# Kernel optimization log

Hardware: AMD Instinct MI355X
Metric: run time of the kernel (lower is better)

Reference implementation:

```python
import jax, jax.numpy as jnp
import numpy as np

TEMP = 0.1
NEG = -1e30  # stands in for removing the diagonal via masked_select
EPS = 1e-12  # F.normalize eps


def _l2norm(x, axis):
    n = jnp.linalg.norm(x, axis=axis, keepdims=True)
    return x / jnp.maximum(n, EPS)


def setup_inputs() -> dict:
    key = jax.random.key(0)
    k = jax.random.split(key, 6)
    B, D = 8192, 128      # instance batch, embed dim
    Bp, P = 256, 256      # patch batch, patches per sample
    v1_ins = jax.random.normal(k[0], (B, D), jnp.float32)
    v2_ins = jax.random.normal(k[1], (B, D), jnp.float32)
    v1_patch = jax.random.normal(k[2], (Bp, D, P), jnp.float32)
    v2_patch = jax.random.normal(k[3], (Bp, D, P), jnp.float32)
    v1_counts = jax.random.randint(k[4], (Bp, P), 0, 50, dtype=jnp.int32)
    v2_counts = jax.random.randint(k[5], (Bp, P), 0, 50, dtype=jnp.int32)
    return {"v1_ins": v1_ins, "v2_ins": v2_ins,
            "v1_patch": v1_patch, "v2_patch": v2_patch,
            "v1_counts": v1_counts, "v2_counts": v2_counts}


def _instance_ce(v1, v2):
    B = v1.shape[0]
    embs = jnp.concatenate([_l2norm(v1, 1), _l2norm(v2, 1)], axis=0)  # [2B, D]
    logits = (embs @ embs.T) / TEMP                                    # [2B, 2B]
    N = 2 * B
    # masking the diagonal to -inf == masked_select removal; positive of row i
    # is column (i+B) mod 2B (matches labels after diagonal removal shift)
    logits = jnp.where(jnp.eye(N, dtype=bool), NEG, logits)
    labels = jnp.concatenate([jnp.arange(B) + B, jnp.arange(B)])
    logp = jax.nn.log_softmax(logits, axis=1)
    return -jnp.mean(logp[jnp.arange(N), labels])


def _patch_ce(v1, v2, c1, c2):
    Bp, D, P = v1.shape
    embs = jnp.concatenate([_l2norm(v1, 1), _l2norm(v2, 1)], axis=2)   # [Bp, D, 2P]
    logits = jnp.einsum('bdi,bdj->bij', embs, embs) / TEMP             # [Bp, 2P, 2P]
    N = 2 * P
    logits = jnp.where(jnp.eye(N, dtype=bool)[None], NEG, logits)
    labels = jnp.concatenate([jnp.arange(P) + P, jnp.arange(P)])       # [2P]
    valid = ~jnp.concatenate([c1 == 0, c2 == 0], axis=1)               # [Bp, 2P]
    logp = jax.nn.log_softmax(logits, axis=2)
    pos = logp[:, jnp.arange(N), labels]                               # [Bp, 2P]
    # ignore_index=-100 -> mean over non-ignored elements
    n_valid = jnp.sum(valid.astype(logits.dtype))
    return -jnp.sum(jnp.where(valid, pos, 0.0)) / n_valid


def reference(v1_ins, v2_ins, v1_patch, v2_patch, v1_counts, v2_counts):
    ins_ce = _instance_ce(v1_ins, v2_ins)
    patch_ce = _patch_ce(v1_patch, v2_patch, v1_counts, v2_counts)
    return ins_ce + patch_ce
```

## Files before the change

### kernel.cpp

```cpp
#include <hip/hip_runtime.h>
#include <math.h>

typedef __bf16 bf16_t;
typedef __bf16 bf16x8 __attribute__((ext_vector_type(8)));
typedef float f32x4 __attribute__((ext_vector_type(4)));
typedef float f32x2 __attribute__((ext_vector_type(2)));

#define B_INS 8192
#define N_INS 16384
#define D 128
#define BP 256
#define P 256
#define NP 512

#define C1_CONST 14.426950408889634f

#define WS_ACC 0
#define WS_S 8
#define WS_POS (8 + 16384)
#define WS_SP (8 + 2 * 16384)
#define WS_PP (WS_SP + BP * NP)
#define WS_ZERO_FLOATS (WS_PP + BP * NP)
#define EMB_I_BYTE ((((WS_ZERO_FLOATS) * 4 + 15) / 16) * 16)
#define EMB_P_BYTE (EMB_I_BYTE + N_INS * D * 2)


#define NB_NORMI 128
#define NB_NORMP 2048
#define NB_ZERO 289
#define NB_PREP (NB_NORMI + NB_NORMP + NB_ZERO)
#define NB_INS 1088
#define NB_PATCHB 1024
#define NB_GRAM (NB_INS + NB_PATCHB)
#define NB_FIN 576

__device__ __forceinline__ void load_lds16(const bf16_t* g, bf16_t* l) {
    __builtin_amdgcn_global_load_lds(
        (const __attribute__((address_space(1))) void*)g,
        (__attribute__((address_space(3))) void*)l, 16, 0, 0);
}

__device__ __forceinline__ void stage_panel(const bf16_t* __restrict__ src,
                                            bf16_t* dst, int w, int lane) {
    const bf16_t* g = src + w * 4096 + lane * 8;
    bf16_t* d = dst + w * 4096;
#pragma unroll
    for (int it = 0; it < 8; it++)
        load_lds16(g + it * 512, d + it * 512);
}

__device__ __forceinline__ void load_afrags(const bf16_t* __restrict__ abase,
                                            int rh, int tx, int q, bf16x8 af[4][4]) {
    const bf16_t* a = abase + ((rh * 64 + tx) << 3);
#pragma unroll
    for (int rt = 0; rt < 4; rt++)
#pragma unroll
        for (int ks = 0; ks < 4; ks++)
            af[rt][ks] = *(const bf16x8*)(a + (((ks << 2) + q) << 10) + (rt << 7));
}

__global__ __launch_bounds__(256) void prep_k(const float* __restrict__ v1i,
                                              const float* __restrict__ v2i,
                                              const float* __restrict__ v1p,
                                              const float* __restrict__ v2p,
                                              bf16_t* __restrict__ embI,
                                              bf16_t* __restrict__ embP,
                                              float* __restrict__ ws) {
    __shared__ float L[128][65];
    __shared__ float ps[4][64];
    __shared__ float invs[128];
    int bx = blockIdx.x;
    int t = threadIdx.x;
    if (bx < NB_NORMI) {
        int p = bx;
        const float* srcP = (p < 64) ? (v1i + (size_t)p * 128 * D)
                                     : (v2i + (size_t)(p - 64) * 128 * D);
        {
            int r = t >> 1, h = t & 1;
            const float* row = srcP + (size_t)r * D + h * 64;
            float ss = 0.f;
#pragma unroll
            for (int j = 0; j < 16; j++) {
                float4 v = *(const float4*)(row + j * 4);
                ss += v.x * v.x + v.y * v.y + v.z * v.z + v.w * v.w;
            }
            ss += __shfl_xor(ss, 1, 64);
            if (h == 0) invs[r] = 1.0f / fmaxf(sqrtf(ss), 1e-12f);
        }
        __syncthreads();
#pragma unroll
        for (int it = 0; it < 8; it++) {
            int idx = it * 256 + t;
            int r = idx & 127, g = idx >> 7;
            const float* src8 = srcP + (size_t)r * D + g * 8;
            float4 a = *(const float4*)(src8);
            float4 b = *(const float4*)(src8 + 4);
            float inv = invs[r];
            bf16x8 v;
            v[0] = (bf16_t)(a.x * inv); v[1] = (bf16_t)(a.y * inv);
            v[2] = (bf16_t)(a.z * inv); v[3] = (bf16_t)(a.w * inv);
            v[4] = (bf16_t)(b.x * inv); v[5] = (bf16_t)(b.y * inv);
            v[6] = (bf16_t)(b.z * inv); v[7] = (bf16_t)(b.w * inv);
            *(bf16x8*)(embI + ((size_t)p << 14) + (g << 10) + (r << 3)) = v;
        }
    } else if (bx < NB_NORMI + NB_NORMP) {
        int bx2 = bx - NB_NORMI;
        int b = bx2 >> 3, h = (bx2 >> 2) & 1, chunk = bx2 & 3;
        int i0 = chunk * 64;
        const float* src = ((h == 0) ? v1p : v2p) + (size_t)b * D * P;
#pragma unroll
        for (int it = 0; it < 8; it++) {
            int fi = it * 256 + t;
            int d = fi >> 4, c4 = fi & 15;
            float4 v = *(const float4*)(src + (size_t)d * P + i0 + c4 * 4);
            L[d][c4 * 4 + 0] = v.x;
            L[d][c4 * 4 + 1] = v.y;
            L[d][c4 * 4 + 2] = v.z;
            L[d][c4 * 4 + 3] = v.w;
        }
        __syncthreads();
        {
            int col = t & 63, part = t >> 6;
            float ss = 0.f;
#pragma unroll 8
            for (int d = part * 32; d < part * 32 + 32; d++) { float x = L[d][col]; ss += x * x; }
            ps[part][col] = ss;
        }
        __syncthreads();
        if (t < 64) {
            float n2 = ps[0][t] + ps[1][t] + ps[2][t] + ps[3][t];
            invs[t] = 1.0f / fmaxf(sqrtf(n2), 1e-12f);
        }
        __syncthreads();
#pragma unroll
        for (int it = 0; it < 4; it++) {
            int idx = it * 256 + t;
            int ic = idx & 63, g = idx >> 6;
            float inv = invs[ic];
            bf16x8 v;
#pragma unroll
            for (int j = 0; j < 8; j++) v[j] = (bf16_t)(L[g * 8 + j][ic] * inv);
            int iLoc = h * P + i0 + ic;
            *(bf16x8*)(embP + ((size_t)b << 16) + ((size_t)(iLoc >> 7) << 14) +
                       (g << 10) + ((iLoc & 127) << 3)) = v;
        }
    } else {
        int idx = (bx - NB_NORMI - NB_NORMP) * 256 + t;
        if (idx < WS_ZERO_FLOATS / 4)
            ((f32x4*)ws)[idx] = (f32x4){0.f, 0.f, 0.f, 0.f};
    }
}

__global__ __launch_bounds__(256) void gram_k(const bf16_t* __restrict__ embI,
                                              const bf16_t* __restrict__ embP,
                                              float* __restrict__ S,
                                              float* __restrict__ pos,
                                              float* __restrict__ Sp,
                                              float* __restrict__ posp) {
    __shared__ __align__(16) bf16_t shB[2][16384];
    int t = threadIdx.x, w = t >> 6, lane = t & 63;
    int tx = lane & 15, q = lane >> 4;
    int rh = w & 1, ch = w >> 1;
    int bx = blockIdx.x;

    const bf16_t *Abase, *Bbase;
    float *Sarr, *posArr;
    int R, c0, n, diagC, posC;
    if (bx < NB_INS) {
        int bid = bx, k = 0, cum = 0;
        while (bid >= cum + 8 * (16 - k)) { cum += 8 * (16 - k); k++; }
        int rem = bid - cum, cc = 16 - k;
        R = 8 * k + rem / cc;
        int ci = rem - (rem / cc) * cc;
        c0 = R + ci * 8;
        n = min(8, 128 - c0);
        Abase = embI + ((size_t)R << 14);
        Bbase = embI;
        Sarr = S; posArr = pos;
        diagC = R; posC = R + 64;
    } else {
        int pi = bx - NB_INS;
        int b = pi >> 2; R = pi & 3;
        c0 = R; n = 4 - R;
        const bf16_t* base = embP + ((size_t)b << 16);
        Abase = base + ((size_t)R << 14);
        Bbase = base;
        Sarr = Sp + (size_t)b * NP; posArr = posp + (size_t)b * NP;
        diagC = R; posC = R + 2;
    }
    int rowBase = R * 128;

    bf16x8 af[4][4];
    load_afrags(Abase, rh, tx, q, af);

    f32x2 rowS2[8];
#pragma unroll
    for (int i = 0; i < 8; i++) rowS2[i] = (f32x2){0.f, 0.f};

    stage_panel(Bbase + ((size_t)c0 << 14), shB[0], w, lane);
    int cur = 0;
    for (int ti = 0; ti < n; ti++) {
        int C = c0 + ti;
        __syncthreads();
        if (ti + 1 < n)
            stage_panel(Bbase + ((size_t)(C + 1) << 14), shB[cur ^ 1], w, lane);
        bool isDiag = (C == diagC), isPos = (C == posC);
        int colBase = C * 128;
        const bf16_t* sb = shB[cur];

        float colS[4];
#pragma unroll
        for (int nt = 0; nt < 4; nt++) {
            bf16x8 bf[4];
#pragma unroll
            for (int ks = 0; ks < 4; ks++)
                bf[ks] = *(const bf16x8*)(sb + (((ks << 2) + q) << 10) +
                                          ((ch * 64 + nt * 16 + tx) << 3));
            f32x4 acc[4];
#pragma unroll
            for (int rt = 0; rt < 4; rt++) acc[rt] = (f32x4){0.f, 0.f, 0.f, 0.f};
#pragma unroll
            for (int ks = 0; ks < 4; ks++)
#pragma unroll
                for (int rt = 0; rt < 4; rt++)
                    acc[rt] = __builtin_amdgcn_mfma_f32_16x16x32_bf16(
                        af[rt][ks], bf[ks], acc[rt], 0, 0, 0);

            f32x2 cs = (f32x2){0.f, 0.f};
#pragma unroll
            for (int rt = 0; rt < 4; rt++) {
                f32x2 l0 = {acc[rt][0], acc[rt][1]};
                f32x2 l1 = {acc[rt][2], acc[rt][3]};
                l0 = l0 * C1_CONST - C1_CONST;
                l1 = l1 * C1_CONST - C1_CONST;
                f32x2 e0 = {__builtin_amdgcn_exp2f(l0.x), __builtin_amdgcn_exp2f(l0.y)};
                f32x2 e1 = {__builtin_amdgcn_exp2f(l1.x), __builtin_amdgcn_exp2f(l1.y)};
                if (isDiag) {
                    int inRow = rh * 64 + rt * 16 + q * 4;
                    int inCol = ch * 64 + nt * 16 + tx;
                    if (inRow + 0 == inCol) e0.x = 0.f;
                    if (inRow + 1 == inCol) e0.y = 0.f;
                    if (inRow + 2 == inCol) e1.x = 0.f;
                    if (inRow + 3 == inCol) e1.y = 0.f;
                }
                rowS2[rt * 2] += e0;
                rowS2[rt * 2 + 1] += e1;
                cs += e0 + e1;
            }
            colS[nt] = cs.x + cs.y;

            if (isPos && ch == rh) {
                int reg = tx - q * 4;
                if (reg >= 0 && reg < 4) {
                    float pl = acc[nt][reg] * 10.0f;
                    atomicAdd(&posArr[rowBase + rh * 64 + nt * 16 + tx], pl);
                    atomicAdd(&posArr[colBase + rh * 64 + nt * 16 + tx], pl);
                }
            }
        }
        if (!isDiag) {
#pragma unroll
            for (int i = 0; i < 4; i++) {
                colS[i] += __shfl_xor(colS[i], 16, 64);
                colS[i] += __shfl_xor(colS[i], 32, 64);
            }
            if (q == 0) {
#pragma unroll
                for (int nt = 0; nt < 4; nt++)
                    atomicAdd(&Sarr[colBase + ch * 64 + nt * 16 + tx], colS[nt]);
            }
        }
        cur ^= 1;
    }
    float* rowS = (float*)rowS2;
#pragma unroll
    for (int off = 1; off <= 8; off <<= 1)
#pragma unroll
        for (int i = 0; i < 16; i++) rowS[i] += __shfl_xor(rowS[i], off, 16);
    if (tx == 0) {
#pragma unroll
        for (int rt = 0; rt < 4; rt++)
#pragma unroll
            for (int reg = 0; reg < 4; reg++)
                atomicAdd(&Sarr[rowBase + rh * 64 + rt * 16 + q * 4 + reg],
                          rowS[rt * 4 + reg]);
    }
}

__global__ __launch_bounds__(256) void fin_k(const float* __restrict__ S,
                                             const float* __restrict__ pos,
                                             const float* __restrict__ Sp,
                                             const float* __restrict__ posp,
                                             const int* __restrict__ c1,
                                             const int* __restrict__ c2,
                                             float* __restrict__ acc,
                                             float* __restrict__ out) {
    int bx = blockIdx.x, t = threadIdx.x;
    int lane = t & 63, w = t >> 6;
    float va = 0.f, nv = 0.f;
    if (bx < 64) {
        int i = bx * 256 + t;
        va = __logf(S[i]) + 10.0f - pos[i];
    } else {
        int idx = (bx - 64) * 256 + t;
        int b = idx >> 9, i = idx & 511;
        int cnt = (i < P) ? c1[b * P + i] : c2[b * P + i - P];
        bool valid = (cnt != 0);
        va = valid ? (__logf(Sp[idx]) + 10.0f - posp[idx]) : 0.f;
        nv = valid ? 1.0f : 0.0f;
    }
#pragma unroll
    for (int off = 32; off >= 1; off >>= 1) {
        va += __shfl_down(va, off, 64);
        nv += __shfl_down(nv, off, 64);
    }
    __shared__ float ps[4], pn[4];
    if (lane == 0) { ps[w] = va; pn[w] = nv; }
    __syncthreads();
    if (t == 0) {
        float sv = ps[0] + ps[1] + ps[2] + ps[3];
        float sn = pn[0] + pn[1] + pn[2] + pn[3];
        if (bx < 64) {
            atomicAdd(&acc[0], sv);
        } else {
            atomicAdd(&acc[1], sv);
            atomicAdd(&acc[2], sn);
        }
        __threadfence();
        unsigned old = atomicAdd((unsigned*)&acc[3], 1u);
        if (old == NB_FIN - 1) {
            float a0 = atomicAdd(&acc[0], 0.0f);
            float a1 = atomicAdd(&acc[1], 0.0f);
            float a2 = atomicAdd(&acc[2], 0.0f);
            out[0] = a0 * (1.0f / (float)N_INS) + a1 / a2;
        }
    }
}

extern "C" void kernel_launch(void* const* d_in, const int* in_sizes, int n_in,
                              void* d_out, int out_size, void* d_ws, size_t ws_size,
                              hipStream_t stream) {
    const float* v1i = (const float*)d_in[0];
    const float* v2i = (const float*)d_in[1];
    const float* v1p = (const float*)d_in[2];
    const float* v2p = (const float*)d_in[3];
    const int* c1 = (const int*)d_in[4];
    const int* c2 = (const int*)d_in[5];
    float* ws = (float*)d_ws;
    float* out = (float*)d_out;
    bf16_t* embI = (bf16_t*)((char*)d_ws + EMB_I_BYTE);
    bf16_t* embP = (bf16_t*)((char*)d_ws + EMB_P_BYTE);

    prep_k<<<NB_PREP, 256, 0, stream>>>(v1i, v2i, v1p, v2p, embI, embP, ws);
    gram_k<<<NB_GRAM, 256, 0, stream>>>(embI, embP, ws + WS_S, ws + WS_POS,
                                        ws + WS_SP, ws + WS_PP);
    fin_k<<<NB_FIN, 256, 0, stream>>>(ws + WS_S, ws + WS_POS, ws + WS_SP,
                                      ws + WS_PP, c1, c2, ws + WS_ACC, out);
}
```

Before: 220.9 us.

## Load B fragments directly from global memory, drop LDS staging and barriers

Removes the double-buffered LDS panel staging and its per-tile __syncthreads, so each wave reads its B fragments straight from global memory (via L2/cache). Adds a launch-bounds occupancy hint of 3 blocks, swizzles the block index so consecutive blocks spread across work regions, and raises wave priority around the MFMA sequence. The aim is to eliminate barrier stalls and raise occupancy now that no LDS is used. The risk is more global-load latency being exposed and redundant B reads across waves that previously shared one LDS copy.

```diff
diff --git a/kernel.cpp b/kernel.cpp
--- a/kernel.cpp
+++ b/kernel.cpp
@@ -33,21 +33,6 @@
 #define NB_PATCHB 1024
 #define NB_GRAM (NB_INS + NB_PATCHB)
 #define NB_FIN 576
-
-__device__ __forceinline__ void load_lds16(const bf16_t* g, bf16_t* l) {
-    __builtin_amdgcn_global_load_lds(
-        (const __attribute__((address_space(1))) void*)g,
-        (__attribute__((address_space(3))) void*)l, 16, 0, 0);
-}
-
-__device__ __forceinline__ void stage_panel(const bf16_t* __restrict__ src,
-                                            bf16_t* dst, int w, int lane) {
-    const bf16_t* g = src + w * 4096 + lane * 8;
-    bf16_t* d = dst + w * 4096;
-#pragma unroll
-    for (int it = 0; it < 8; it++)
-        load_lds16(g + it * 512, d + it * 512);
-}
 
 __device__ __forceinline__ void load_afrags(const bf16_t* __restrict__ abase,
                                             int rh, int tx, int q, bf16x8 af[4][4]) {
@@ -151,17 +136,17 @@
     }
 }
 
-__global__ __launch_bounds__(256) void gram_k(const bf16_t* __restrict__ embI,
-                                              const bf16_t* __restrict__ embP,
-                                              float* __restrict__ S,
-                                              float* __restrict__ pos,
-                                              float* __restrict__ Sp,
-                                              float* __restrict__ posp) {
-    __shared__ __align__(16) bf16_t shB[2][16384];
+__global__ __launch_bounds__(256, 3) void gram_k(const bf16_t* __restrict__ embI,
+                                                 const bf16_t* __restrict__ embP,
+                                                 float* __restrict__ S,
+                                                 float* __restrict__ pos,
+                                                 float* __restrict__ Sp,
+                                                 float* __restrict__ posp) {
     int t = threadIdx.x, w = t >> 6, lane = t & 63;
     int tx = lane & 15, q = lane >> 4;
     int rh = w & 1, ch = w >> 1;
-    int bx = blockIdx.x;
+    int bx0 = blockIdx.x;
+    int bx = (bx0 & 7) * (NB_GRAM / 8) + (bx0 >> 3);
 
     const bf16_t *Abase, *Bbase;
     float *Sarr, *posArr;
@@ -197,16 +182,13 @@
 #pragma unroll
     for (int i = 0; i < 8; i++) rowS2[i] = (f32x2){0.f, 0.f};
 
-    stage_panel(Bbase + ((size_t)c0 << 14), shB[0], w, lane);
-    int cur = 0;
+    const bf16_t* bcol = Bbase + ((size_t)q << 10) + ((ch * 64 + tx) << 3);
+
     for (int ti = 0; ti < n; ti++) {
         int C = c0 + ti;
-        __syncthreads();
-        if (ti + 1 < n)
-            stage_panel(Bbase + ((size_t)(C + 1) << 14), shB[cur ^ 1], w, lane);
         bool isDiag = (C == diagC), isPos = (C == posC);
         int colBase = C * 128;
-        const bf16_t* sb = shB[cur];
+        const bf16_t* pb = bcol + ((size_t)C << 14);
 
         float colS[4];
 #pragma unroll
@@ -214,17 +196,18 @@
             bf16x8 bf[4];
 #pragma unroll
             for (int ks = 0; ks < 4; ks++)
-                bf[ks] = *(const bf16x8*)(sb + (((ks << 2) + q) << 10) +
-                                          ((ch * 64 + nt * 16 + tx) << 3));
+                bf[ks] = *(const bf16x8*)(pb + (ks << 12) + (nt << 7));
             f32x4 acc[4];
 #pragma unroll
             for (int rt = 0; rt < 4; rt++) acc[rt] = (f32x4){0.f, 0.f, 0.f, 0.f};
+            __builtin_amdgcn_s_setprio(1);
 #pragma unroll
             for (int ks = 0; ks < 4; ks++)
 #pragma unroll
                 for (int rt = 0; rt < 4; rt++)
                     acc[rt] = __builtin_amdgcn_mfma_f32_16x16x32_bf16(
                         af[rt][ks], bf[ks], acc[rt], 0, 0, 0);
+            __builtin_amdgcn_s_setprio(0);
 
             f32x2 cs = (f32x2){0.f, 0.f};
 #pragma unroll
@@ -270,7 +253,6 @@
                     atomicAdd(&Sarr[colBase + ch * 64 + nt * 16 + tx], colS[nt]);
             }
         }
-        cur ^= 1;
     }
     float* rowS = (float*)rowS2;
 #pragma unroll
```

Result: slower. 236.1 us (+6.9%).

## Replace global atomic row/column sum accumulation with per-tile partial buffers

Applied to the files above, without the earlier changes.

Instead of atomically adding row and column exp-sums into shared global arrays, each gram tile now writes its partial sums into a dedicated slot. The finalize kernel then reduces these partials per row. This removes atomic contention and the large workspace zeroing in the prep kernel. In exchange it needs more workspace traffic and longer serial reduction loops in the finalize kernel.

```diff
diff --git a/kernel.cpp b/kernel.cpp
--- a/kernel.cpp
+++ b/kernel.cpp
@@ -16,23 +16,25 @@
 #define C1_CONST 14.426950408889634f
 
 #define WS_ACC 0
-#define WS_S 8
-#define WS_POS (8 + 16384)
-#define WS_SP (8 + 2 * 16384)
-#define WS_PP (WS_SP + BP * NP)
-#define WS_ZERO_FLOATS (WS_PP + BP * NP)
-#define EMB_I_BYTE ((((WS_ZERO_FLOATS) * 4 + 15) / 16) * 16)
+#define WS_POS 8
+#define WS_PPOS (WS_POS + N_INS)
+#define NPAIRI 8128
+#define WS_CI (WS_PPOS + BP * NP)
+#define WS_RI (WS_CI + NPAIRI * 256)
+#define WS_CP (WS_RI + 1088 * 256)
+#define WS_RP (WS_CP + BP * 6 * 256)
+#define WS_END (WS_RP + 1024 * 256)
+#define EMB_I_BYTE ((((WS_END) * 4 + 15) / 16) * 16)
 #define EMB_P_BYTE (EMB_I_BYTE + N_INS * D * 2)
 
 
 #define NB_NORMI 128
 #define NB_NORMP 2048
-#define NB_ZERO 289
-#define NB_PREP (NB_NORMI + NB_NORMP + NB_ZERO)
+#define NB_PREP (NB_NORMI + NB_NORMP + 1)
 #define NB_INS 1088
 #define NB_PATCHB 1024
 #define NB_GRAM (NB_INS + NB_PATCHB)
-#define NB_FIN 576
+#define NB_FIN (128 + 256)
 
 __device__ __forceinline__ void load_lds16(const bf16_t* g, bf16_t* l) {
     __builtin_amdgcn_global_load_lds(
@@ -145,18 +147,18 @@
                        (g << 10) + ((iLoc & 127) << 3)) = v;
         }
     } else {
-        int idx = (bx - NB_NORMI - NB_NORMP) * 256 + t;
-        if (idx < WS_ZERO_FLOATS / 4)
-            ((f32x4*)ws)[idx] = (f32x4){0.f, 0.f, 0.f, 0.f};
+        if (t < 8) ws[t] = 0.f;
     }
 }
 
 __global__ __launch_bounds__(256) void gram_k(const bf16_t* __restrict__ embI,
                                               const bf16_t* __restrict__ embP,
-                                              float* __restrict__ S,
                                               float* __restrict__ pos,
-                                              float* __restrict__ Sp,
-                                              float* __restrict__ posp) {
+                                              float* __restrict__ posp,
+                                              float* __restrict__ colI,
+                                              float* __restrict__ rowI,
+                                              float* __restrict__ colP,
+                                              float* __restrict__ rowP) {
     __shared__ __align__(16) bf16_t shB[2][16384];
     int t = threadIdx.x, w = t >> 6, lane = t & 63;
     int tx = lane & 15, q = lane >> 4;
@@ -164,7 +166,7 @@
     int bx = blockIdx.x;
 
     const bf16_t *Abase, *Bbase;
-    float *Sarr, *posArr;
+    float *posArr, *colArr, *rowDst;
     int R, c0, n, diagC, posC;
     if (bx < NB_INS) {
         int bid = bx, k = 0, cum = 0;
@@ -176,7 +178,9 @@
         n = min(8, 128 - c0);
         Abase = embI + ((size_t)R << 14);
         Bbase = embI;
-        Sarr = S; posArr = pos;
+        posArr = pos;
+        colArr = colI + (size_t)R * 256;
+        rowDst = rowI + (size_t)(R * 16 + ci) * 256;
         diagC = R; posC = R + 64;
     } else {
         int pi = bx - NB_INS;
@@ -185,7 +189,9 @@
         const bf16_t* base = embP + ((size_t)b << 16);
         Abase = base + ((size_t)R << 14);
         Bbase = base;
-        Sarr = Sp + (size_t)b * NP; posArr = posp + (size_t)b * NP;
+        posArr = posp + (size_t)b * NP;
+        colArr = colP + (size_t)(b * 6 + R) * 256;
+        rowDst = rowP + (size_t)((b << 2) + R) * 256;
         diagC = R; posC = R + 2;
     }
     int rowBase = R * 128;
@@ -253,8 +259,8 @@
                 int reg = tx - q * 4;
                 if (reg >= 0 && reg < 4) {
                     float pl = acc[nt][reg] * 10.0f;
-                    atomicAdd(&posArr[rowBase + rh * 64 + nt * 16 + tx], pl);
-                    atomicAdd(&posArr[colBase + rh * 64 + nt * 16 + tx], pl);
+                    posArr[rowBase + rh * 64 + nt * 16 + tx] = pl;
+                    posArr[colBase + rh * 64 + nt * 16 + tx] = pl;
                 }
             }
         }
@@ -265,9 +271,10 @@
                 colS[i] += __shfl_xor(colS[i], 32, 64);
             }
             if (q == 0) {
+                float* cdst = colArr + (size_t)(C * (C - 1) / 2) * 256 + rh * 128;
 #pragma unroll
                 for (int nt = 0; nt < 4; nt++)
-                    atomicAdd(&Sarr[colBase + ch * 64 + nt * 16 + tx], colS[nt]);
+                    cdst[ch * 64 + nt * 16 + tx] = colS[nt];
             }
         }
         cur ^= 1;
@@ -282,15 +289,17 @@
         for (int rt = 0; rt < 4; rt++)
 #pragma unroll
             for (int reg = 0; reg < 4; reg++)
-                atomicAdd(&Sarr[rowBase + rh * 64 + rt * 16 + q * 4 + reg],
-                          rowS[rt * 4 + reg]);
-    }
-}
-
-__global__ __launch_bounds__(256) void fin_k(const float* __restrict__ S,
-                                             const float* __restrict__ pos,
-                                             const float* __restrict__ Sp,
+                rowDst[ch * 128 + rh * 64 + rt * 16 + q * 4 + reg] =
+                    rowS[rt * 4 + reg];
+    }
+}
+
+__global__ __launch_bounds__(256) void fin_k(const float* __restrict__ pos,
                                              const float* __restrict__ posp,
+                                             const float* __restrict__ colI,
+                                             const float* __restrict__ rowI,
+                                             const float* __restrict__ colP,
+                                             const float* __restrict__ rowP,
                                              const int* __restrict__ c1,
                                              const int* __restrict__ c2,
                                              float* __restrict__ acc,
@@ -298,29 +307,51 @@
     int bx = blockIdx.x, t = threadIdx.x;
     int lane = t & 63, w = t >> 6;
     float va = 0.f, nv = 0.f;
-    if (bx < 64) {
-        int i = bx * 256 + t;
-        va = __logf(S[i]) + 10.0f - pos[i];
+    __shared__ float comb[128];
+    if (bx < 128) {
+        int p = bx;
+        int half = t >> 7, r = t & 127;
+        int cc = 16 - (p >> 3);
+        float s = 0.f;
+        const float* RIp = rowI + (size_t)(p * 16) * 256 + half * 128 + r;
+        for (int ci = 0; ci < cc; ci++) s += RIp[ci * 256];
+        const float* CIp = colI + (size_t)(p * (p - 1) / 2) * 256 + half * 128 + r;
+        for (int Rq = 0; Rq < p; Rq++) s += CIp[Rq * 256];
+        if (half == 1) comb[r] = s;
+        __syncthreads();
+        if (half == 0) {
+            float S = s + comb[r];
+            va = __logf(S) + 10.0f - pos[p * 128 + r];
+        }
     } else {
-        int idx = (bx - 64) * 256 + t;
-        int b = idx >> 9, i = idx & 511;
-        int cnt = (i < P) ? c1[b * P + i] : c2[b * P + i - P];
-        bool valid = (cnt != 0);
-        va = valid ? (__logf(Sp[idx]) + 10.0f - posp[idx]) : 0.f;
-        nv = valid ? 1.0f : 0.0f;
+        int b = bx - 128;
+#pragma unroll
+        for (int it = 0; it < 2; it++) {
+            int idx = it * 256 + t;
+            int p = idx >> 7, r = idx & 127;
+            const float* RPp = rowP + (size_t)((b << 2) + p) * 256 + r;
+            float s = RPp[0] + RPp[128];
+            const float* CPp = colP + (size_t)(b * 6 + p * (p - 1) / 2) * 256 + r;
+            for (int Rq = 0; Rq < p; Rq++) s += CPp[Rq * 256] + CPp[Rq * 256 + 128];
+            int cnt = (idx < P) ? c1[b * P + idx] : c2[b * P + idx - P];
+            if (cnt != 0) {
+                va += __logf(s) + 10.0f - posp[b * NP + idx];
+                nv += 1.0f;
+            }
+        }
     }
 #pragma unroll
     for (int off = 32; off >= 1; off >>= 1) {
         va += __shfl_down(va, off, 64);
         nv += __shfl_down(nv, off, 64);
     }
-    __shared__ float ps[4], pn[4];
-    if (lane == 0) { ps[w] = va; pn[w] = nv; }
+    __shared__ float psum[4], pn[4];
+    if (lane == 0) { psum[w] = va; pn[w] = nv; }
     __syncthreads();
     if (t == 0) {
-        float sv = ps[0] + ps[1] + ps[2] + ps[3];
+        float sv = psum[0] + psum[1] + psum[2] + psum[3];
         float sn = pn[0] + pn[1] + pn[2] + pn[3];
-        if (bx < 64) {
+        if (bx < 128) {
             atomicAdd(&acc[0], sv);
         } else {
             atomicAdd(&acc[1], sv);
@@ -352,8 +383,10 @@
     bf16_t* embP = (bf16_t*)((char*)d_ws + EMB_P_BYTE);
 
     prep_k<<<NB_PREP, 256, 0, stream>>>(v1i, v2i, v1p, v2p, embI, embP, ws);
-    gram_k<<<NB_GRAM, 256, 0, stream>>>(embI, embP, ws + WS_S, ws + WS_POS,
-                                        ws + WS_SP, ws + WS_PP);
-    fin_k<<<NB_FIN, 256, 0, stream>>>(ws + WS_S, ws + WS_POS, ws + WS_SP,
-                                      ws + WS_PP, c1, c2, ws + WS_ACC, out);
-}
+    gram_k<<<NB_GRAM, 256, 0, stream>>>(embI, embP, ws + WS_POS, ws + WS_PPOS,
+                                        ws + WS_CI, ws + WS_RI,
+                                        ws + WS_CP, ws + WS_RP);
+    fin_k<<<NB_FIN, 256, 0, stream>>>(ws + WS_POS, ws + WS_PPOS, ws + WS_CI,
+                                      ws + WS_RI, ws + WS_CP, ws + WS_RP,
+                                      c1, c2, ws + WS_ACC, out);
+}
```

Result: slower. 226.5 us (+2.5%).
